# Optimization experiments

Hardware: AMD Instinct MI355X
Metric: run time of the kernel (lower is better)

## Reference

```python
import jax, jax.numpy as jnp
import numpy as np

D_MODEL = 1024
N_HEADS = 16
HEAD_DIM = D_MODEL // N_HEADS


def _linear_params(key, fan_in, fan_out):
    kw, kb = jax.random.split(key)
    bound = 1.0 / np.sqrt(fan_in)
    W = jax.random.uniform(kw, (fan_in, fan_out), jnp.float32, -bound, bound)
    b = jax.random.uniform(kb, (fan_out,), jnp.float32, -bound, bound)
    return W, b


def setup_inputs() -> dict:
    key = jax.random.key(0)
    ks = jax.random.split(key, 7)
    B, N = 4, 2048
    q = jax.random.normal(ks[0], (B, N, D_MODEL), jnp.float32)
    k = jax.random.normal(ks[1], (B, N, D_MODEL), jnp.float32)
    v = jax.random.normal(ks[2], (B, N, D_MODEL), jnp.float32)
    Wq, bq = _linear_params(ks[3], D_MODEL, D_MODEL)
    Wk, bk = _linear_params(ks[4], D_MODEL, D_MODEL)
    Wv, bv = _linear_params(ks[5], D_MODEL, D_MODEL)
    Wo, bo = _linear_params(ks[6], D_MODEL, D_MODEL)
    return {"q": q, "k": k, "v": v,
            "Wq": Wq, "bq": bq, "Wk": Wk, "bk": bk,
            "Wv": Wv, "bv": bv, "Wo": Wo, "bo": bo}


def reference(q, k, v, Wq, bq, Wk, bk, Wv, bv, Wo, bo):
    B, N, _ = q.shape
    # fused QKV projection + head split: [B, N, D] -> [B, H, N, hd]
    def split_heads(x):
        return x.reshape(B, N, N_HEADS, HEAD_DIM).transpose(0, 2, 1, 3)
    qh = split_heads(q @ Wq + bq)
    kh = split_heads(k @ Wk + bk)
    vh = split_heads(v @ Wv + bv)
    # scaled dot-product attention (mask=None)
    scale = 1.0 / np.sqrt(HEAD_DIM)
    scores = jnp.einsum('bhqd,bhkd->bhqk', qh, kh) * scale  # [B,H,N,N]
    attn_weights = jax.nn.softmax(scores, axis=-1)
    attn_out = jnp.einsum('bhqk,bhkd->bhqd', attn_weights, vh)
    # merge heads: [B,H,N,hd] -> [B,N,D]
    attn_out = attn_out.transpose(0, 2, 1, 3).reshape(B, N, D_MODEL)
    output = attn_out @ Wo + bo
    return output, attn_weights
```

## Files before the change

### kernel.cpp

```cpp
#include <hip/hip_runtime.h>
#include <hip/hip_bf16.h>
#include <stdint.h>

#define D_MODEL 1024
#define NH      16
#define HD      64
#define B_SZ    4
#define SEQ     2048
#define M_TOT   (B_SZ*SEQ)
#define LOG2E_O8 0.18033688011112042f

typedef __bf16 bf16;
typedef bf16  bf16x8 __attribute__((ext_vector_type(8)));
typedef bf16  bf16x4 __attribute__((ext_vector_type(4)));
typedef float f32x4  __attribute__((ext_vector_type(4)));

static __device__ __forceinline__ f32x4 mfma16(bf16x8 a, bf16x8 b, f32x4 c) {
  return __builtin_amdgcn_mfma_f32_16x16x32_bf16(a, b, c, 0, 0, 0);
}

static __device__ __forceinline__ void gl2lds(const void* g, void* l) {
  __builtin_amdgcn_global_load_lds(
      (const __attribute__((address_space(1))) unsigned int*)g,
      (__attribute__((address_space(3))) unsigned int*)l,
      16, 0, 0);
}

#define BAR_VM16() do { \
  asm volatile("s_waitcnt vmcnt(16) lgkmcnt(0)" ::: "memory"); \
  __builtin_amdgcn_s_barrier(); \
  __builtin_amdgcn_sched_barrier(0); \
} while (0)

#define BAR_LGKM() do { \
  asm volatile("s_waitcnt lgkmcnt(0)" ::: "memory"); \
  __builtin_amdgcn_s_barrier(); \
  __builtin_amdgcn_sched_barrier(0); \
} while (0)

__global__ __launch_bounds__(256) void k_twt(const float* __restrict__ w0,
                                             const float* __restrict__ w1,
                                             const float* __restrict__ w2,
                                             const float* __restrict__ w3,
                                             bf16* __restrict__ t0,
                                             bf16* __restrict__ t1,
                                             bf16* __restrict__ t2,
                                             bf16* __restrict__ t3) {
  __shared__ bf16 t[64][65];
  int z = blockIdx.z;
  const float* W = z == 0 ? w0 : z == 1 ? w1 : z == 2 ? w2 : w3;
  bf16* Wt = z == 0 ? t0 : z == 1 ? t1 : z == 2 ? t2 : t3;
  int k0 = blockIdx.x * 64, n0 = blockIdx.y * 64;
  int r = threadIdx.x >> 2, c0 = (threadIdx.x & 3) * 16;
  const float* p = W + (size_t)(k0 + r) * D_MODEL + n0 + c0;
#pragma unroll
  for (int e = 0; e < 16; e += 4) {
    float4 v = *(const float4*)(p + e);
    t[r][c0+e+0] = (bf16)v.x; t[r][c0+e+1] = (bf16)v.y;
    t[r][c0+e+2] = (bf16)v.z; t[r][c0+e+3] = (bf16)v.w;
  }
  __syncthreads();
  bf16x8 o0, o1;
#pragma unroll
  for (int e = 0; e < 8; e++) { o0[e] = t[c0+e][r]; o1[e] = t[c0+8+e][r]; }
  bf16* q = Wt + (size_t)(n0 + r) * D_MODEL + k0 + c0;
  *(bf16x8*)q = o0; *(bf16x8*)(q + 8) = o1;
}

__global__ __launch_bounds__(256) void k_qkv(const float* __restrict__ Aq,
                                             const float* __restrict__ Ak,
                                             const float* __restrict__ Av,
                                             const bf16* __restrict__ Wt3,
                                             const float* __restrict__ bq,
                                             const float* __restrict__ bk,
                                             const float* __restrict__ bv,
                                             bf16* __restrict__ HQ,
                                             bf16* __restrict__ Vt) {
  __shared__ alignas(16) bf16 sA[2][8192];
  __shared__ alignas(16) bf16 sB[2][8192];
  const int tid = threadIdx.x;
  const int lane = tid & 63, wv = tid >> 6;
  const int g = lane >> 4, lr = lane & 15;
  const int wm = wv >> 1, wn = wv & 1;
  const int d = blockIdx.x;
  const int p = (d & 7) * 24 + (d >> 6);
  const int seg = p >> 6;
  const int m0 = (p & 63) * 128;
  const int n0 = ((d >> 3) & 7) * 128;

  const float* A = seg == 0 ? Aq : seg == 1 ? Ak : Av;
  const float* bias = seg == 0 ? bq : seg == 1 ? bk : bv;
  const float oscale = seg == 0 ? LOG2E_O8 : 1.0f;

  const float* ap[4]; int adst[4];
#pragma unroll
  for (int i = 0; i < 4; i++) {
    int row = i * 32 + (tid >> 3), col = (tid & 7) * 8;
    ap[i] = A + (size_t)(m0 + row) * D_MODEL + col;
    adst[i] = row * 128 + ((col * 2) ^ ((row & 7) << 4));
  }
  const char* bsrc[4]; int bdst[4];
#pragma unroll
  for (int i = 0; i < 4; i++) {
    int o = i * 4096 + tid * 16;
    int brow = o >> 7, bin = o & 127;
    bsrc[i] = (const char*)Wt3 + (size_t)(seg * 1024 + n0 + brow) * 2048
              + (bin ^ ((brow & 7) << 4));
    bdst[i] = i * 4096 + wv * 1024;
  }
  int fa[4], fb[4], swa[4], swb[4];
#pragma unroll
  for (int i = 0; i < 4; i++) {
    int rowa = wm * 64 + i * 16 + lr;
    int rowb = wn * 64 + i * 16 + lr;
    fa[i] = rowa * 128; swa[i] = (rowa & 7) << 4;
    fb[i] = rowb * 128; swb[i] = (rowb & 7) << 4;
  }
  f32x4 acc[4][4] = {};
  float4 af[4][2];

#pragma unroll
  for (int i = 0; i < 4; i++) gl2lds(bsrc[i], (char*)sB[0] + bdst[i]);
#pragma unroll
  for (int i = 0; i < 4; i++) { af[i][0] = *(const float4*)ap[i]; af[i][1] = *(const float4*)(ap[i] + 4); }
#pragma unroll
  for (int i = 0; i < 4; i++) {
    bf16x8 w8;
#pragma unroll
    for (int e = 0; e < 4; e++) { w8[e] = (bf16)af[i][0][e]; w8[4+e] = (bf16)af[i][1][e]; }
    *(bf16x8*)((char*)sA[0] + adst[i]) = w8;
  }
  __syncthreads();

  int cur = 0;
  for (int kt = 0; kt < 16; ++kt) {
    if (kt < 15) {
#pragma unroll
      for (int i = 0; i < 4; i++)
        gl2lds(bsrc[i] + (kt + 1) * 128, (char*)sB[cur ^ 1] + bdst[i]);
#pragma unroll
      for (int i = 0; i < 4; i++) {
        af[i][0] = *(const float4*)(ap[i] + (kt + 1) * 64);
        af[i][1] = *(const float4*)(ap[i] + (kt + 1) * 64 + 4);
      }
    }
    const char* bA = (const char*)sA[cur];
    const char* bB = (const char*)sB[cur];
#pragma unroll
    for (int c = 0; c < 2; c++) {
      bf16x8 a[4], b[4];
      int off = c * 64 + g * 16;
#pragma unroll
      for (int i = 0; i < 4; i++) {
        a[i] = *(const bf16x8*)(bA + fa[i] + (off ^ swa[i]));
        b[i] = *(const bf16x8*)(bB + fb[i] + (off ^ swb[i]));
      }
#pragma unroll
      for (int mi = 0; mi < 4; mi++)
#pragma unroll
        for (int ni = 0; ni < 4; ni++)
          acc[mi][ni] = mfma16(a[mi], b[ni], acc[mi][ni]);
    }
    if (kt < 15) {
#pragma unroll
      for (int i = 0; i < 4; i++) {
        bf16x8 w8;
#pragma unroll
        for (int e = 0; e < 4; e++) { w8[e] = (bf16)af[i][0][e]; w8[4+e] = (bf16)af[i][1][e]; }
        *(bf16x8*)((char*)sA[cur ^ 1] + adst[i]) = w8;
      }
    }
    __syncthreads();
    cur ^= 1;
  }

  if (seg < 2) {
    bf16* outp = HQ + (size_t)seg * 8388608;
#pragma unroll
    for (int mi = 0; mi < 4; mi++) {
#pragma unroll
      for (int ni = 0; ni < 4; ni++) {
        int n = n0 + wn * 64 + ni * 16 + lr;
        float bvl = bias[n];
        int h = n >> 6, dd = n & 63;
#pragma unroll
        for (int r = 0; r < 4; r++) {
          int m = m0 + wm * 64 + mi * 16 + g * 4 + r;
          int b = m >> 11, q = m & 2047;
          outp[(((size_t)(b * NH + h)) * SEQ + q) * HD + dd] =
              (bf16)((acc[mi][ni][r] + bvl) * oscale);
        }
      }
    }
  } else {
    char* tr = (char*)sA;
#pragma unroll
    for (int mi = 0; mi < 4; mi++) {
#pragma unroll
      for (int ni = 0; ni < 4; ni++) {
        int n_loc = wn * 64 + ni * 16 + lr;
        float bvl = bias[n0 + n_loc];
        bf16x4 pq;
#pragma unroll
        for (int r = 0; r < 4; r++) pq[r] = (bf16)(acc[mi][ni][r] + bvl);
        int m0l = wm * 64 + mi * 16 + g * 4;
        *(bf16x4*)(tr + n_loc * 256 + ((m0l * 2) ^ ((n_loc & 7) << 4))) = pq;
      }
    }
    __syncthreads();
    int n_loc = tid >> 1, mh = (tid & 1) * 64;
    int n_glob = n0 + n_loc;
    int h = n_glob >> 6, dd = n_glob & 63;
    int b = m0 >> 11, q0l = (m0 & 2047) + mh;
    bf16* vp = Vt + ((size_t)(b * NH + h) * HD + dd) * SEQ + q0l;
    int sw = (n_loc & 7) << 4;
#pragma unroll
    for (int c = 0; c < 8; c++) {
      bf16x8 v8 = *(const bf16x8*)(tr + n_loc * 256 + ((mh * 2 + c * 16) ^ sw));
      *(bf16x8*)(vp + c * 8) = v8;
    }
  }
}

__global__ __launch_bounds__(256) void k_ogemm(const bf16* __restrict__ A,
                                               const bf16* __restrict__ Bt,
                                               const float* __restrict__ bias,
                                               float* __restrict__ outp) {
  __shared__ alignas(16) bf16 sA[2][8192];
  __shared__ alignas(16) bf16 sB[2][8192];
  const int tid = threadIdx.x;
  const int lane = tid & 63, wv = tid >> 6;
  const int g = lane >> 4, lr = lane & 15;
  const int wm = wv >> 1, wn = wv & 1;
  const int d = blockIdx.x;
  const int m0 = ((d & 7) * 8 + (d >> 6)) * 128;
  const int n0 = ((d >> 3) & 7) * 128;

  const char* asrc[4]; const char* bsrc[4]; int dst[4];
#pragma unroll
  for (int i = 0; i < 4; i++) {
    int o = i * 4096 + tid * 16;
    int row = o >> 7, in = o & 127;
    int cs = in ^ ((row & 7) << 4);
    asrc[i] = (const char*)A  + (size_t)(m0 + row) * 2048 + cs;
    bsrc[i] = (const char*)Bt + (size_t)(n0 + row) * 2048 + cs;
    dst[i] = i * 4096 + wv * 1024;
  }
  int fa[4], fb[4], swa[4], swb[4];
#pragma unroll
  for (int i = 0; i < 4; i++) {
    int rowa = wm * 64 + i * 16 + lr;
    int rowb = wn * 64 + i * 16 + lr;
    fa[i] = rowa * 128; swa[i] = (rowa & 7) << 4;
    fb[i] = rowb * 128; swb[i] = (rowb & 7) << 4;
  }
  f32x4 acc[4][4] = {};
#pragma unroll
  for (int i = 0; i < 4; i++) {
    gl2lds(asrc[i], (char*)sA[0] + dst[i]);
    gl2lds(bsrc[i], (char*)sB[0] + dst[i]);
  }
  __syncthreads();
  int cur = 0;
  for (int kt = 0; kt < 16; ++kt) {
    if (kt < 15) {
#pragma unroll
      for (int i = 0; i < 4; i++) {
        gl2lds(asrc[i] + (kt + 1) * 128, (char*)sA[cur ^ 1] + dst[i]);
        gl2lds(bsrc[i] + (kt + 1) * 128, (char*)sB[cur ^ 1] + dst[i]);
      }
    }
    const char* bA = (const char*)sA[cur];
    const char* bB = (const char*)sB[cur];
#pragma unroll
    for (int c = 0; c < 2; c++) {
      bf16x8 a[4], b[4];
      int off = c * 64 + g * 16;
#pragma unroll
      for (int i = 0; i < 4; i++) {
        a[i] = *(const bf16x8*)(bA + fa[i] + (off ^ swa[i]));
        b[i] = *(const bf16x8*)(bB + fb[i] + (off ^ swb[i]));
      }
#pragma unroll
      for (int mi = 0; mi < 4; mi++)
#pragma unroll
        for (int ni = 0; ni < 4; ni++)
          acc[mi][ni] = mfma16(a[mi], b[ni], acc[mi][ni]);
    }
    __syncthreads();
    cur ^= 1;
  }
#pragma unroll
  for (int mi = 0; mi < 4; mi++) {
#pragma unroll
    for (int ni = 0; ni < 4; ni++) {
      int n = n0 + wn * 64 + ni * 16 + lr;
      float bvl = bias[n];
#pragma unroll
      for (int r = 0; r < 4; r++) {
        int m = m0 + wm * 64 + mi * 16 + g * 4 + r;
        outp[(size_t)m * D_MODEL + n] = acc[mi][ni][r] + bvl;
      }
    }
  }
}

__global__ __launch_bounds__(256) void k_attn(const bf16* __restrict__ Qh,
                                              const bf16* __restrict__ Kh,
                                              const bf16* __restrict__ Vt,
                                              float* __restrict__ Wout,
                                              bf16* __restrict__ O) {
  __shared__ alignas(16) bf16 sK[2][8192];
  __shared__ alignas(16) bf16 sV[8192];
  __shared__ alignas(16) bf16 sP[16384];
  const int tid = threadIdx.x, lane = tid & 63, wv = tid >> 6;
  const int g = lane >> 4, lr = lane & 15;
  int swzb = (blockIdx.x & 7) * 64 + (blockIdx.x >> 3);
  const int bh = swzb >> 3;
  const int qt0 = (swzb & 7) * 256;
  const int qw0 = qt0 + wv * 32;
  const int qw1 = qt0 + 128 + wv * 32;

  bf16x8 qb0[2][2], qb1[2][2];
#pragma unroll
  for (int mi = 0; mi < 2; mi++)
#pragma unroll
    for (int c = 0; c < 2; c++) {
      qb0[mi][c] = *(const bf16x8*)(Qh + ((size_t)bh * SEQ + qw0 + mi * 16 + lr) * HD + c * 32 + g * 8);
      qb1[mi][c] = *(const bf16x8*)(Qh + ((size_t)bh * SEQ + qw1 + mi * 16 + lr) * HD + c * 32 + g * 8);
    }

  const char* kbase = (const char*)(Kh + (size_t)bh * SEQ * HD);
  const char* vbase = (const char*)(Vt + (size_t)bh * HD * SEQ);
  const char* ksrc[4]; const char* vsrc[4]; int ldst[4];
#pragma unroll
  for (int i = 0; i < 4; i++) {
    int o = i * 4096 + tid * 16;
    int kr = o >> 7, kin = o & 127;
    ksrc[i] = kbase + (size_t)kr * 128 + (kin ^ ((kr & 7) << 4));
    int dr = o >> 8, vin = o & 255;
    vsrc[i] = vbase + (size_t)dr * 4096 + (vin ^ ((dr & 7) << 4));
    ldst[i] = i * 4096 + wv * 1024;
  }

#pragma unroll
  for (int i = 0; i < 4; i++) gl2lds(ksrc[i], (char*)sK + ldst[i]);
  __syncthreads();

  float rsum0[2] = {0.f, 0.f};
  int cur = 0;
  for (int kt = 0; kt < 16; ++kt) {
    int nx = ((kt + 1) & 15) * 16384;
#pragma unroll
    for (int i = 0; i < 4; i++)
      gl2lds(ksrc[i] + nx, (char*)sK + (cur ^ 1) * 16384 + ldst[i]);
    const char* kb = (char*)sK + cur * 16384;
#pragma unroll
    for (int nf = 0; nf < 8; nf++) {
      int krow = nf * 16 + lr, sw = (krow & 7) << 4;
      bf16x8 k0 = *(const bf16x8*)(kb + krow * 128 + ((g * 16) ^ sw));
      bf16x8 k1 = *(const bf16x8*)(kb + krow * 128 + ((64 + g * 16) ^ sw));
#pragma unroll
      for (int mi = 0; mi < 2; mi++) {
        f32x4 t = {};
        t = mfma16(k0, qb0[mi][0], t);
        t = mfma16(k1, qb0[mi][1], t);
        rsum0[mi] += __builtin_amdgcn_exp2f(t[0]) + __builtin_amdgcn_exp2f(t[1])
                   + __builtin_amdgcn_exp2f(t[2]) + __builtin_amdgcn_exp2f(t[3]);
      }
    }
    __syncthreads();
    cur ^= 1;
  }
  float lrl0[2];
#pragma unroll
  for (int mi = 0; mi < 2; mi++) {
    float s = rsum0[mi];
    s += __shfl_xor(s, 16); s += __shfl_xor(s, 32);
    lrl0[mi] = -__builtin_amdgcn_logf(s);
  }
  const int osrc0 = (lane >> 3) + 16 * (lane & 3);
  const int osrc1 = 8 + (lane >> 3) + 16 * (lane & 3);
  const bool selhi = (lane >> 2) & 1;
  float* wrow0[2][2]; float* wrow1[2][2];
#pragma unroll
  for (int mi = 0; mi < 2; mi++)
#pragma unroll
    for (int h = 0; h < 2; h++) {
      wrow0[mi][h] = Wout + ((size_t)bh * SEQ + qw0 + mi * 16 + 8 * h + (lane >> 3)) * SEQ
                     + 4 * (lane & 7);
      wrow1[mi][h] = Wout + ((size_t)bh * SEQ + qw1 + mi * 16 + 8 * h + (lane >> 3)) * SEQ
                     + 4 * (lane & 7);
    }

  float rsum1[2] = {0.f, 0.f};
  f32x4 oc0[2][4] = {};
  for (int kt = 0; kt < 16; ++kt) {
#pragma unroll
    for (int i = 0; i < 4; i++) {
      gl2lds(ksrc[i] + ((kt + 1) & 15) * 16384, (char*)sK + (cur ^ 1) * 16384 + ldst[i]);
      gl2lds(vsrc[i] + kt * 256, (char*)sV + ldst[i]);
    }
    const char* kb = (char*)sK + cur * 16384;
#pragma unroll
    for (int mi = 0; mi < 2; mi++) {
      f32x4 wreg[8];
#pragma unroll
      for (int nf = 0; nf < 8; nf++) {
        int krow = nf * 16 + lr, sw = (krow & 7) << 4;
        bf16x8 k0 = *(const bf16x8*)(kb + krow * 128 + ((g * 16) ^ sw));
        bf16x8 k1 = *(const bf16x8*)(kb + krow * 128 + ((64 + g * 16) ^ sw));
        f32x4 t = {};
        t = mfma16(k0, qb0[mi][0], t);
        t = mfma16(k1, qb0[mi][1], t);
        f32x4 w4;
        w4[0] = __builtin_amdgcn_exp2f(t[0] + lrl0[mi]);
        w4[1] = __builtin_amdgcn_exp2f(t[1] + lrl0[mi]);
        w4[2] = __builtin_amdgcn_exp2f(t[2] + lrl0[mi]);
        w4[3] = __builtin_amdgcn_exp2f(t[3] + lrl0[mi]);
        wreg[nf] = w4;
        bf16x4 p4;
        p4[0] = (bf16)w4[0]; p4[1] = (bf16)w4[1]; p4[2] = (bf16)w4[2]; p4[3] = (bf16)w4[3];
        int lq = wv * 32 + mi * 16 + lr;
        *(bf16x4*)((char*)sP + lq * 256 + (((nf * 16 + g * 4) * 2) ^ ((lq & 7) << 4))) = p4;
      }
#pragma unroll
      for (int h = 0; h < 2; h++) {
        int osrc = h ? osrc1 : osrc0;
#pragma unroll
        for (int c = 0; c < 4; c++) {
          f32x4 va, vb, outv;
#pragma unroll
          for (int e = 0; e < 4; e++) {
            va[e] = __shfl(wreg[2 * c][e], osrc);
            vb[e] = __shfl(wreg[2 * c + 1][e], osrc);
          }
#pragma unroll
          for (int e = 0; e < 4; e++) outv[e] = selhi ? vb[e] : va[e];
          __builtin_nontemporal_store(outv,
              (f32x4*)(wrow0[mi][h] + kt * 128 + 32 * c));
        }
      }
    }
#pragma unroll
    for (int nf = 0; nf < 8; nf++) {
      int krow = nf * 16 + lr, sw = (krow & 7) << 4;
      bf16x8 k0 = *(const bf16x8*)(kb + krow * 128 + ((g * 16) ^ sw));
      bf16x8 k1 = *(const bf16x8*)(kb + krow * 128 + ((64 + g * 16) ^ sw));
#pragma unroll
      for (int mi = 0; mi < 2; mi++) {
        f32x4 t = {};
        t = mfma16(k0, qb1[mi][0], t);
        t = mfma16(k1, qb1[mi][1], t);
        rsum1[mi] += __builtin_amdgcn_exp2f(t[0]) + __builtin_amdgcn_exp2f(t[1])
                   + __builtin_amdgcn_exp2f(t[2]) + __builtin_amdgcn_exp2f(t[3]);
      }
    }
    BAR_VM16();
#pragma unroll
    for (int c = 0; c < 4; c++) {
      bf16x8 pa[2];
#pragma unroll
      for (int mi = 0; mi < 2; mi++) {
        int lq = wv * 32 + mi * 16 + lr;
        pa[mi] = *(const bf16x8*)((char*)sP + lq * 256 + ((c * 64 + g * 16) ^ ((lq & 7) << 4)));
      }
#pragma unroll
      for (int df = 0; df < 4; df++) {
        int dr = df * 16 + lr;
        bf16x8 vb2 = *(const bf16x8*)((char*)sV + dr * 256 + ((c * 64 + g * 16) ^ ((dr & 7) << 4)));
#pragma unroll
        for (int mi = 0; mi < 2; mi++)
          oc0[mi][df] = mfma16(pa[mi], vb2, oc0[mi][df]);
      }
    }
    BAR_LGKM();
    cur ^= 1;
  }
  float lrl1[2];
#pragma unroll
  for (int mi = 0; mi < 2; mi++) {
    float s = rsum1[mi];
    s += __shfl_xor(s, 16); s += __shfl_xor(s, 32);
    lrl1[mi] = -__builtin_amdgcn_logf(s);
  }
  {
    int b = bh >> 4, h = bh & 15;
#pragma unroll
    for (int mi = 0; mi < 2; mi++)
#pragma unroll
      for (int df = 0; df < 4; df++)
#pragma unroll
        for (int r = 0; r < 4; r++) {
          int q = qw0 + mi * 16 + g * 4 + r;
          int dd = df * 16 + lr;
          O[((size_t)(b * SEQ + q) * NH + h) * HD + dd] = (bf16)oc0[mi][df][r];
        }
  }

  f32x4 oc1[2][4] = {};
  for (int kt = 0; kt < 16; ++kt) {
#pragma unroll
    for (int i = 0; i < 4; i++) {
      if (kt < 15)
        gl2lds(ksrc[i] + (kt + 1) * 16384, (char*)sK + (cur ^ 1) * 16384 + ldst[i]);
      gl2lds(vsrc[i] + kt * 256, (char*)sV + ldst[i]);
    }
    const char* kb = (char*)sK + cur * 16384;
#pragma unroll
    for (int mi = 0; mi < 2; mi++) {
      f32x4 wreg[8];
#pragma unroll
      for (int nf = 0; nf < 8; nf++) {
        int krow = nf * 16 + lr, sw = (krow & 7) << 4;
        bf16x8 k0 = *(const bf16x8*)(kb + krow * 128 + ((g * 16) ^ sw));
        bf16x8 k1 = *(const bf16x8*)(kb + krow * 128 + ((64 + g * 16) ^ sw));
        f32x4 t = {};
        t = mfma16(k0, qb1[mi][0], t);
        t = mfma16(k1, qb1[mi][1], t);
        f32x4 w4;
        w4[0] = __builtin_amdgcn_exp2f(t[0] + lrl1[mi]);
        w4[1] = __builtin_amdgcn_exp2f(t[1] + lrl1[mi]);
        w4[2] = __builtin_amdgcn_exp2f(t[2] + lrl1[mi]);
        w4[3] = __builtin_amdgcn_exp2f(t[3] + lrl1[mi]);
        wreg[nf] = w4;
        bf16x4 p4;
        p4[0] = (bf16)w4[0]; p4[1] = (bf16)w4[1]; p4[2] = (bf16)w4[2]; p4[3] = (bf16)w4[3];
        int lq = wv * 32 + mi * 16 + lr;
        *(bf16x4*)((char*)sP + lq * 256 + (((nf * 16 + g * 4) * 2) ^ ((lq & 7) << 4))) = p4;
      }
#pragma unroll
      for (int h = 0; h < 2; h++) {
        int osrc = h ? osrc1 : osrc0;
#pragma unroll
        for (int c = 0; c < 4; c++) {
          f32x4 va, vb, outv;
#pragma unroll
          for (int e = 0; e < 4; e++) {
            va[e] = __shfl(wreg[2 * c][e], osrc);
            vb[e] = __shfl(wreg[2 * c + 1][e], osrc);
          }
#pragma unroll
          for (int e = 0; e < 4; e++) outv[e] = selhi ? vb[e] : va[e];
          __builtin_nontemporal_store(outv,
              (f32x4*)(wrow1[mi][h] + kt * 128 + 32 * c));
        }
      }
    }
    BAR_VM16();
#pragma unroll
    for (int c = 0; c < 4; c++) {
      bf16x8 pa[2];
#pragma unroll
      for (int mi = 0; mi < 2; mi++) {
        int lq = wv * 32 + mi * 16 + lr;
        pa[mi] = *(const bf16x8*)((char*)sP + lq * 256 + ((c * 64 + g * 16) ^ ((lq & 7) << 4)));
      }
#pragma unroll
      for (int df = 0; df < 4; df++) {
        int dr = df * 16 + lr;
        bf16x8 vb2 = *(const bf16x8*)((char*)sV + dr * 256 + ((c * 64 + g * 16) ^ ((dr & 7) << 4)));
#pragma unroll
        for (int mi = 0; mi < 2; mi++)
          oc1[mi][df] = mfma16(pa[mi], vb2, oc1[mi][df]);
      }
    }
    BAR_LGKM();
    cur ^= 1;
  }
  {
    int b = bh >> 4, h = bh & 15;
#pragma unroll
    for (int mi = 0; mi < 2; mi++)
#pragma unroll
      for (int df = 0; df < 4; df++)
#pragma unroll
        for (int r = 0; r < 4; r++) {
          int q = qw1 + mi * 16 + g * 4 + r;
          int dd = df * 16 + lr;
          O[((size_t)(b * SEQ + q) * NH + h) * HD + dd] = (bf16)oc1[mi][df][r];
        }
  }
}

extern "C" void kernel_launch(void* const* d_in, const int* in_sizes, int n_in,
                              void* d_out, int out_size, void* d_ws, size_t ws_size,
                              hipStream_t stream) {
  const float* q  = (const float*)d_in[0];
  const float* k  = (const float*)d_in[1];
  const float* v  = (const float*)d_in[2];
  const float* Wq = (const float*)d_in[3];
  const float* bq = (const float*)d_in[4];
  const float* Wk = (const float*)d_in[5];
  const float* bk = (const float*)d_in[6];
  const float* Wv = (const float*)d_in[7];
  const float* bv = (const float*)d_in[8];
  const float* Wo = (const float*)d_in[9];
  const float* bo = (const float*)d_in[10];

  char* ws = (char*)d_ws;
  bf16* Obuf = (bf16*)(ws);
  bf16* Wt3  = (bf16*)(ws + 16777216);
  bf16* WtO  = (bf16*)(ws + 16777216 + 3 * 2097152);
  bf16* HQ   = (bf16*)(ws + 25165824);
  bf16* Kh   = (bf16*)(ws + 41943040);
  bf16* Vt   = (bf16*)(ws + 75497472);

  float* out0 = (float*)d_out;
  float* wout = out0 + (size_t)M_TOT * D_MODEL;

  dim3 blk(256);
  k_twt<<<dim3(16, 16, 4), blk, 0, stream>>>(Wq, Wk, Wv, Wo,
                                             Wt3, Wt3 + 1048576, Wt3 + 2097152, WtO);
  k_qkv<<<dim3(1536), blk, 0, stream>>>(q, k, v, Wt3, bq, bk, bv, HQ, Vt);
  k_attn<<<dim3(512), blk, 0, stream>>>(HQ, Kh, Vt, wout, Obuf);
  k_ogemm<<<dim3(512), blk, 0, stream>>>(Obuf, WtO, bo, out0);
}
```

Before: 372.9 us.

## Widen QKV GEMM tile to 128x256 with triple-buffered K=32 pipeline

Rewrites the QKV projection kernel to use 128x256 output tiles, which halves the grid and doubles per-wave MFMA work (4x8 fragments). K steps drop to 32 wide and use a three-stage LDS ring with one barrier per step, along with a new row-pair swizzle and launch bounds for two blocks per CU. The aim is more reuse of each A tile, since every fp32 A row is loaded and converted half as often, and better overlap of loads with MFMA. In exchange the kernel uses more registers and LDS (72KB), which may limit occupancy, and the V transpose epilogue is adjusted to the wider tile.

```diff
diff --git a/kernel.cpp b/kernel.cpp
--- a/kernel.cpp
+++ b/kernel.cpp
@@ -37,6 +37,10 @@
   __builtin_amdgcn_s_barrier(); \
   __builtin_amdgcn_sched_barrier(0); \
 } while (0)
+
+static __device__ __forceinline__ int lds_off(int r, int kb) {
+  return ((r >> 1) << 7) + ((((r & 1) << 6) + kb) ^ (((r >> 1) & 7) << 4));
+}
 
 __global__ __launch_bounds__(256) void k_twt(const float* __restrict__ w0,
                                              const float* __restrict__ w1,
@@ -67,111 +71,104 @@
   *(bf16x8*)q = o0; *(bf16x8*)(q + 8) = o1;
 }
 
-__global__ __launch_bounds__(256) void k_qkv(const float* __restrict__ Aq,
-                                             const float* __restrict__ Ak,
-                                             const float* __restrict__ Av,
-                                             const bf16* __restrict__ Wt3,
-                                             const float* __restrict__ bq,
-                                             const float* __restrict__ bk,
-                                             const float* __restrict__ bv,
-                                             bf16* __restrict__ HQ,
-                                             bf16* __restrict__ Vt) {
-  __shared__ alignas(16) bf16 sA[2][8192];
-  __shared__ alignas(16) bf16 sB[2][8192];
+__global__ __launch_bounds__(256, 2) void k_qkv8(const float* __restrict__ Aq,
+                                                 const float* __restrict__ Ak,
+                                                 const float* __restrict__ Av,
+                                                 const bf16* __restrict__ Wt3,
+                                                 const float* __restrict__ bq,
+                                                 const float* __restrict__ bk,
+                                                 const float* __restrict__ bv,
+                                                 bf16* __restrict__ HQ,
+                                                 bf16* __restrict__ Vt) {
+  __shared__ alignas(16) char smem[73728];
   const int tid = threadIdx.x;
   const int lane = tid & 63, wv = tid >> 6;
   const int g = lane >> 4, lr = lane & 15;
   const int wm = wv >> 1, wn = wv & 1;
-  const int d = blockIdx.x;
-  const int p = (d & 7) * 24 + (d >> 6);
-  const int seg = p >> 6;
-  const int m0 = (p & 63) * 128;
-  const int n0 = ((d >> 3) & 7) * 128;
+  const int dd = blockIdx.x;
+  const int P = (dd & 7) * 96 + (dd >> 3);
+  const int seg = P >> 8;
+  const int rem = P & 255;
+  const int m0 = (rem >> 2) * 128;
+  const int n0 = (rem & 3) * 256;
 
   const float* A = seg == 0 ? Aq : seg == 1 ? Ak : Av;
   const float* bias = seg == 0 ? bq : seg == 1 ? bk : bv;
   const float oscale = seg == 0 ? LOG2E_O8 : 1.0f;
 
-  const float* ap[4]; int adst[4];
-#pragma unroll
-  for (int i = 0; i < 4; i++) {
-    int row = i * 32 + (tid >> 3), col = (tid & 7) * 8;
-    ap[i] = A + (size_t)(m0 + row) * D_MODEL + col;
-    adst[i] = row * 128 + ((col * 2) ^ ((row & 7) << 4));
-  }
+  const float* aptr = A + (size_t)(m0 + (tid >> 1)) * D_MODEL + (tid & 1) * 16;
+  const int awoff0 = lds_off(tid >> 1, (tid & 1) * 32);
+  const int awoff1 = lds_off(tid >> 1, (tid & 1) * 32 + 16);
   const char* bsrc[4]; int bdst[4];
 #pragma unroll
-  for (int i = 0; i < 4; i++) {
-    int o = i * 4096 + tid * 16;
-    int brow = o >> 7, bin = o & 127;
-    bsrc[i] = (const char*)Wt3 + (size_t)(seg * 1024 + n0 + brow) * 2048
-              + (bin ^ ((brow & 7) << 4));
-    bdst[i] = i * 4096 + wv * 1024;
-  }
-  int fa[4], fb[4], swa[4], swb[4];
-#pragma unroll
-  for (int i = 0; i < 4; i++) {
-    int rowa = wm * 64 + i * 16 + lr;
-    int rowb = wn * 64 + i * 16 + lr;
-    fa[i] = rowa * 128; swa[i] = (rowa & 7) << 4;
-    fb[i] = rowb * 128; swb[i] = (rowb & 7) << 4;
-  }
-  f32x4 acc[4][4] = {};
-  float4 af[4][2];
-
-#pragma unroll
-  for (int i = 0; i < 4; i++) gl2lds(bsrc[i], (char*)sB[0] + bdst[i]);
-#pragma unroll
-  for (int i = 0; i < 4; i++) { af[i][0] = *(const float4*)ap[i]; af[i][1] = *(const float4*)(ap[i] + 4); }
-#pragma unroll
-  for (int i = 0; i < 4; i++) {
-    bf16x8 w8;
-#pragma unroll
-    for (int e = 0; e < 4; e++) { w8[e] = (bf16)af[i][0][e]; w8[4+e] = (bf16)af[i][1][e]; }
-    *(bf16x8*)((char*)sA[0] + adst[i]) = w8;
-  }
-  __syncthreads();
-
-  int cur = 0;
-  for (int kt = 0; kt < 16; ++kt) {
-    if (kt < 15) {
-#pragma unroll
-      for (int i = 0; i < 4; i++)
-        gl2lds(bsrc[i] + (kt + 1) * 128, (char*)sB[cur ^ 1] + bdst[i]);
-#pragma unroll
-      for (int i = 0; i < 4; i++) {
-        af[i][0] = *(const float4*)(ap[i] + (kt + 1) * 64);
-        af[i][1] = *(const float4*)(ap[i] + (kt + 1) * 64 + 4);
-      }
-    }
-    const char* bA = (const char*)sA[cur];
-    const char* bB = (const char*)sB[cur];
-#pragma unroll
-    for (int c = 0; c < 2; c++) {
-      bf16x8 a[4], b[4];
-      int off = c * 64 + g * 16;
-#pragma unroll
-      for (int i = 0; i < 4; i++) {
-        a[i] = *(const bf16x8*)(bA + fa[i] + (off ^ swa[i]));
-        b[i] = *(const bf16x8*)(bB + fb[i] + (off ^ swb[i]));
-      }
-#pragma unroll
-      for (int mi = 0; mi < 4; mi++)
-#pragma unroll
-        for (int ni = 0; ni < 4; ni++)
-          acc[mi][ni] = mfma16(a[mi], b[ni], acc[mi][ni]);
-    }
-    if (kt < 15) {
-#pragma unroll
-      for (int i = 0; i < 4; i++) {
-        bf16x8 w8;
-#pragma unroll
-        for (int e = 0; e < 4; e++) { w8[e] = (bf16)af[i][0][e]; w8[4+e] = (bf16)af[i][1][e]; }
-        *(bf16x8*)((char*)sA[cur ^ 1] + adst[i]) = w8;
-      }
-    }
-    __syncthreads();
-    cur ^= 1;
+  for (int u = 0; u < 4; u++) {
+    int o = u * 4096 + tid * 16;
+    int p = o >> 7, w = o & 127;
+    int wq = w ^ ((p & 7) << 4);
+    int r = p * 2 + (wq >> 6), kb = wq & 63;
+    bsrc[u] = (const char*)(Wt3 + (size_t)(seg * 1024 + n0 + r) * D_MODEL) + kb;
+    bdst[u] = o;
+  }
+  int aoff[4], boff[8];
+#pragma unroll
+  for (int mi = 0; mi < 4; mi++) aoff[mi] = lds_off(wm * 64 + mi * 16 + lr, g * 16);
+#pragma unroll
+  for (int ni = 0; ni < 8; ni++) boff[ni] = lds_off(wn * 128 + ni * 16 + lr, g * 16);
+
+  f32x4 acc[4][8] = {};
+  float4 af[4];
+
+#pragma unroll
+  for (int j = 0; j < 4; j++) af[j] = *(const float4*)(aptr + j * 4);
+#pragma unroll
+  for (int u = 0; u < 4; u++) gl2lds(bsrc[u], smem + 24576 + bdst[u]);
+  asm volatile("s_waitcnt vmcnt(0)" ::: "memory");
+  {
+    bf16x8 w8a, w8b;
+#pragma unroll
+    for (int e = 0; e < 4; e++) {
+      w8a[e] = (bf16)af[0][e]; w8a[4+e] = (bf16)af[1][e];
+      w8b[e] = (bf16)af[2][e]; w8b[4+e] = (bf16)af[3][e];
+    }
+    *(bf16x8*)(smem + awoff0) = w8a;
+    *(bf16x8*)(smem + awoff1) = w8b;
+  }
+
+  int bufc = 0;
+  for (int s = 0; s < 32; ++s) {
+    int kn = (s + 1) & 31;
+    int nxt = bufc + 1; if (nxt == 3) nxt = 0;
+#pragma unroll
+    for (int j = 0; j < 4; j++) af[j] = *(const float4*)(aptr + kn * 32 + j * 4);
+#pragma unroll
+    for (int u = 0; u < 4; u++)
+      gl2lds(bsrc[u] + kn * 64, smem + 24576 + nxt * 16384 + bdst[u]);
+    asm volatile("s_waitcnt vmcnt(8) lgkmcnt(0)" ::: "memory");
+    __builtin_amdgcn_s_barrier();
+    __builtin_amdgcn_sched_barrier(0);
+    const char* bA = smem + bufc * 8192;
+    const char* bB = smem + 24576 + bufc * 16384;
+    bf16x8 a[4], b[8];
+#pragma unroll
+    for (int mi = 0; mi < 4; mi++) a[mi] = *(const bf16x8*)(bA + aoff[mi]);
+#pragma unroll
+    for (int ni = 0; ni < 8; ni++) b[ni] = *(const bf16x8*)(bB + boff[ni]);
+#pragma unroll
+    for (int mi = 0; mi < 4; mi++)
+#pragma unroll
+      for (int ni = 0; ni < 8; ni++)
+        acc[mi][ni] = mfma16(a[mi], b[ni], acc[mi][ni]);
+    {
+      bf16x8 w8a, w8b;
+#pragma unroll
+      for (int e = 0; e < 4; e++) {
+        w8a[e] = (bf16)af[0][e]; w8a[4+e] = (bf16)af[1][e];
+        w8b[e] = (bf16)af[2][e]; w8b[4+e] = (bf16)af[3][e];
+      }
+      *(bf16x8*)(smem + nxt * 8192 + awoff0) = w8a;
+      *(bf16x8*)(smem + nxt * 8192 + awoff1) = w8b;
+    }
+    bufc = nxt;
   }
 
   if (seg < 2) {
@@ -179,26 +176,27 @@
 #pragma unroll
     for (int mi = 0; mi < 4; mi++) {
 #pragma unroll
-      for (int ni = 0; ni < 4; ni++) {
-        int n = n0 + wn * 64 + ni * 16 + lr;
+      for (int ni = 0; ni < 8; ni++) {
+        int n = n0 + wn * 128 + ni * 16 + lr;
         float bvl = bias[n];
-        int h = n >> 6, dd = n & 63;
+        int h = n >> 6, dcol = n & 63;
 #pragma unroll
         for (int r = 0; r < 4; r++) {
           int m = m0 + wm * 64 + mi * 16 + g * 4 + r;
-          int b = m >> 11, q = m & 2047;
-          outp[(((size_t)(b * NH + h)) * SEQ + q) * HD + dd] =
+          int b2 = m >> 11, q = m & 2047;
+          outp[(((size_t)(b2 * NH + h)) * SEQ + q) * HD + dcol] =
               (bf16)((acc[mi][ni][r] + bvl) * oscale);
         }
       }
     }
   } else {
-    char* tr = (char*)sA;
+    __syncthreads();
+    char* tr = smem;
 #pragma unroll
     for (int mi = 0; mi < 4; mi++) {
 #pragma unroll
-      for (int ni = 0; ni < 4; ni++) {
-        int n_loc = wn * 64 + ni * 16 + lr;
+      for (int ni = 0; ni < 8; ni++) {
+        int n_loc = wn * 128 + ni * 16 + lr;
         float bvl = bias[n0 + n_loc];
         bf16x4 pq;
 #pragma unroll
@@ -208,15 +206,15 @@
       }
     }
     __syncthreads();
-    int n_loc = tid >> 1, mh = (tid & 1) * 64;
+    int n_loc = tid;
     int n_glob = n0 + n_loc;
-    int h = n_glob >> 6, dd = n_glob & 63;
-    int b = m0 >> 11, q0l = (m0 & 2047) + mh;
-    bf16* vp = Vt + ((size_t)(b * NH + h) * HD + dd) * SEQ + q0l;
+    int h = n_glob >> 6, dcol = n_glob & 63;
+    int b2 = m0 >> 11, q0l = m0 & 2047;
+    bf16* vp = Vt + ((size_t)(b2 * NH + h) * HD + dcol) * SEQ + q0l;
     int sw = (n_loc & 7) << 4;
 #pragma unroll
-    for (int c = 0; c < 8; c++) {
-      bf16x8 v8 = *(const bf16x8*)(tr + n_loc * 256 + ((mh * 2 + c * 16) ^ sw));
+    for (int c = 0; c < 16; c++) {
+      bf16x8 v8 = *(const bf16x8*)(tr + n_loc * 256 + ((c * 16) ^ sw));
       *(bf16x8*)(vp + c * 8) = v8;
     }
   }
@@ -493,8 +491,8 @@
 #pragma unroll
         for (int r = 0; r < 4; r++) {
           int q = qw0 + mi * 16 + g * 4 + r;
-          int dd = df * 16 + lr;
-          O[((size_t)(b * SEQ + q) * NH + h) * HD + dd] = (bf16)oc0[mi][df][r];
+          int dcol = df * 16 + lr;
+          O[((size_t)(b * SEQ + q) * NH + h) * HD + dcol] = (bf16)oc0[mi][df][r];
         }
   }
 
@@ -577,8 +575,8 @@
 #pragma unroll
         for (int r = 0; r < 4; r++) {
           int q = qw1 + mi * 16 + g * 4 + r;
-          int dd = df * 16 + lr;
-          O[((size_t)(b * SEQ + q) * NH + h) * HD + dd] = (bf16)oc1[mi][df][r];
+          int dcol = df * 16 + lr;
+          O[((size_t)(b * SEQ + q) * NH + h) * HD + dcol] = (bf16)oc1[mi][df][r];
         }
   }
 }
@@ -612,7 +610,7 @@
   dim3 blk(256);
   k_twt<<<dim3(16, 16, 4), blk, 0, stream>>>(Wq, Wk, Wv, Wo,
                                              Wt3, Wt3 + 1048576, Wt3 + 2097152, WtO);
-  k_qkv<<<dim3(1536), blk, 0, stream>>>(q, k, v, Wt3, bq, bk, bv, HQ, Vt);
+  k_qkv8<<<dim3(768), blk, 0, stream>>>(q, k, v, Wt3, bq, bk, bv, HQ, Vt);
   k_attn<<<dim3(512), blk, 0, stream>>>(HQ, Kh, Vt, wout, Obuf);
   k_ogemm<<<dim3(512), blk, 0, stream>>>(Obuf, WtO, bo, out0);
 }
```

After: 348.0 us (median of 2 runs). -6.7%, faster.
